# Kernel optimization log

Measured on AMD Instinct MI355X. Metric: run time of the kernel, lower is better.

## Reference

```python
import jax, jax.numpy as jnp
import numpy as np

H = 128; L = 4; N_TOTAL = 2500; M = 4; K = 12
S = N_TOTAL * M          # 10000 subgraphs
F = S * K                # 120000 flat nodes
E_INTRA = 2 * F          # 240000 intra-subgraph edges
E_INTER = 16 * N_TOTAL   # 40000 canonical edges
B = 50; VOCAB = 119; MAX_DIST = 32; BN_EPS = 1e-5


def _bn(x, g, b):
    # training-mode BatchNorm1d over rows (biased var, eps=1e-5)
    mu = x.mean(0)
    var = x.var(0)
    return (x - mu) * jax.lax.rsqrt(var + BN_EPS) * g + b


def _gine(x, ei, ea, W1, b1, W2, b2):
    # PyG GINEConv, eps=0: MLP(x + sum_{src->dst} relu(x[src] + e))
    msg = jax.nn.relu(x[ei[0]] + ea)                              # [E,H]
    agg = jax.ops.segment_sum(msg, ei[1], num_segments=x.shape[0])
    h = x + agg
    return jax.nn.relu(h @ W1 + b1) @ W2 + b2


def setup_inputs():
    key = jax.random.key(0)
    ks = list(jax.random.split(key, 32)); it = iter(ks)
    nk = lambda: next(it)
    rn = lambda shape, s=0.05: jax.random.normal(nk(), shape, dtype=jnp.float32) * s
    x_tok = jax.random.randint(nk(), (F,), 0, VOCAB)
    dist = jax.random.randint(nk(), (F,), 0, MAX_DIST + 1)
    node_ids = jax.random.randint(nk(), (F,), 0, N_TOTAL)
    node_ids = jnp.where(jax.random.uniform(nk(), (F,)) < 0.1, -1, node_ids)
    root_flat_idx = jnp.arange(S) * K
    node_ids = node_ids.at[root_flat_idx].set(jnp.arange(S) // M)  # root = canonical node
    valid = node_ids >= 0
    sub_batch = jnp.repeat(jnp.arange(S), K)
    src = jax.random.randint(nk(), (E_INTRA,), 0, F)
    dst = (src // K) * K + jax.random.randint(nk(), (E_INTRA,), 0, K)  # stay inside subgraph
    intra_ei = jnp.stack([src, dst])
    edge_index = jax.random.randint(nk(), (2, E_INTER), 0, N_TOTAL)
    batch_ids = jnp.arange(N_TOTAL) // (N_TOTAL // B)
    lp = -jax.random.uniform(nk(), (S,)) * 3.0                    # log-probs <= 0
    z = lambda *shape: jnp.zeros(shape, jnp.float32)
    o = lambda *shape: jnp.ones(shape, jnp.float32)
    return dict(
        x_tok=x_tok, dist=dist, node_ids=node_ids, valid=valid,
        sub_batch=sub_batch, root_flat_idx=root_flat_idx,
        intra_ei=intra_ei, edge_index=edge_index, batch_ids=batch_ids,
        lp=lp, ea_flat=rn((E_INTRA, H)), edge_attr=rn((E_INTER, H)),
        atom_emb=rn((VOCAB, H)), dist_emb=rn((MAX_DIST + 1, H)),
        logp_w=rn((1, H)), logp_b=z(H),
        intra_W1=rn((L, H, H)), intra_b1=z(L, H),
        intra_W2=rn((L, H, H)), intra_b2=z(L, H),
        intra_bn_g=o(L, H), intra_bn_b=z(L, H),
        self_W=rn((L, H, H)), self_b=z(L, H),
        root_W=rn((L, H, H)), root_b=z(L, H),
        inter_W1=rn((L, H, H)), inter_b1=z(L, H),
        inter_W2=rn((L, H, H)), inter_b2=z(L, H),
        inter_bn_g=o(L, H), inter_bn_b=z(L, H),
        readout_bn_g=o(H), readout_bn_b=z(H),
        alpha_pool=o(1), alpha_inter=o(1),
    )


def reference(x_tok, dist, node_ids, valid, sub_batch, root_flat_idx, intra_ei,
              edge_index, batch_ids, lp, ea_flat, edge_attr, atom_emb, dist_emb,
              logp_w, logp_b, intra_W1, intra_b1, intra_W2, intra_b2,
              intra_bn_g, intra_bn_b, self_W, self_b, root_W, root_b,
              inter_W1, inter_b1, inter_W2, inter_b2, inter_bn_g, inter_bn_b,
              readout_bn_g, readout_bn_b, alpha_pool, alpha_inter):
    valid_f = valid.astype(jnp.float32)[:, None]                  # [F,1]
    is_root_f = jnp.zeros((F, 1), jnp.float32).at[root_flat_idx].set(1.0)
    clamped_ids = jnp.maximum(node_ids, 0)
    # input encoding: atom embedding + BFS-distance PE + log-prob PE
    logp_pe = jax.nn.relu(lp[sub_batch][:, None] * logp_w[0] + logp_b)
    h = (atom_emb[x_tok] + dist_emb[dist] + logp_pe) * valid_f
    # HT inter-root weights, normalized per canonical root id
    root_ids = node_ids[root_flat_idx]                            # [S]
    rv = root_ids >= 0
    rid = jnp.maximum(root_ids, 0)
    w_un = jnp.where(rv, jnp.exp(-alpha_inter[0] * lp), 0.0)
    w_sum = jax.ops.segment_sum(w_un, rid, num_segments=N_TOTAL)
    ht_w = jnp.where(rv, w_un / (w_sum[rid] + 1e-16), 0.0)        # [S]
    for l in range(L):
        h1 = _gine(h, intra_ei, ea_flat, intra_W1[l], intra_b1[l], intra_W2[l], intra_b2[l])
        h1 = _bn(h1, intra_bn_g[l], intra_bn_b[l]) * valid_f
        h_root_bcast = h[sub_batch * K]
        h_non_root = (h @ self_W[l] + self_b[l]) + (h_root_bcast @ root_W[l] + root_b[l])
        # HT-weighted scatter of root reps to canonical nodes
        h_roots = h[root_flat_idx]                                # [S,H]
        h_root_canon = jax.ops.segment_sum(h_roots * ht_w[:, None], rid, num_segments=N_TOTAL)
        h_inter = _gine(h_root_canon, edge_index, edge_attr, inter_W1[l], inter_b1[l], inter_W2[l], inter_b2[l])
        h_inter = _bn(h_inter, inter_bn_g[l], inter_bn_b[l])
        h_inter_bcast = h_inter[clamped_ids] * valid_f
        out = is_root_f * (h1 + h_inter_bcast) + (1.0 - is_root_f) * (h1 + h_non_root)
        h = jax.nn.relu(out) * valid_f                            # dropout p=0
    # HT softmax readout over the m subgraphs of each canonical node
    h_sub = jax.ops.segment_sum(h * valid_f, sub_batch, num_segments=S)
    h_sub_2d = h_sub.reshape(N_TOTAL, M, H)
    w = jax.nn.softmax(-alpha_pool[0] * lp.reshape(N_TOTAL, M), axis=1)
    node_emb = jnp.einsum('nm,nmh->nh', w, h_sub_2d)
    node_emb = _bn(node_emb, readout_bn_g, readout_bn_b)
    return jax.ops.segment_sum(node_emb, batch_ids, num_segments=B)  # [B,H]
```

## Files before the change

### kernel.cpp

```cpp
#include <hip/hip_runtime.h>
#include <math.h>

#define H 128
#define H4 (H/4)
#define KK 12
#define MSUB 4
#define FF 120000
#define SS 10000
#define NN 2500
#define NBATCH 50
#define NLAYER 4
#define EINTRA 240000
#define EINTER 40000
#define HH (H*H)
#define BN_EPS 1e-5f
#define CAP_I 32
#define CAP_E 96

typedef short short8 __attribute__((ext_vector_type(8)));
typedef float floatx4 __attribute__((ext_vector_type(4)));

__device__ __forceinline__ unsigned short f2bf_rne(float x){
  unsigned u = __float_as_uint(x);
  unsigned r = u + 0x7FFFu + ((u >> 16) & 1u);
  return (unsigned short)(r >> 16);
}


__global__ void k_zero(float* __restrict__ p, int n){
  int i = blockIdx.x*256 + threadIdx.x;
  if (i < n) p[i] = 0.f;
}

__global__ void k_zeroi(int* __restrict__ p, int n){
  int i = blockIdx.x*256 + threadIdx.x;
  if (i < n) p[i] = 0;
}


__global__ void k_bucket(const int* __restrict__ dst, int E, int* __restrict__ cnt,
                         int* __restrict__ beid, int cap){
  int e = blockIdx.x*256 + threadIdx.x;
  if (e >= E) return;
  int d = dst[e];
  int p = atomicAdd(&cnt[d], 1);
  if (p < cap) beid[(size_t)d*cap + p] = e;
}

__global__ void k_scan(const int* __restrict__ cnt, int rows, int cap,
                       int* __restrict__ rowptr, int* __restrict__ gcount){
  __shared__ int sdata[256];
  __shared__ int sbase;
  int tid = threadIdx.x;
  int r = blockIdx.x*256 + tid;
  int v = 0;
  if (r < rows){ v = cnt[r]; if (v > cap) v = cap; }
  sdata[tid] = v;
  __syncthreads();
  for (int ofs = 1; ofs < 256; ofs <<= 1){
    int t = (tid >= ofs) ? sdata[tid-ofs] : 0;
    __syncthreads();
    sdata[tid] += t;
    __syncthreads();
  }
  if (tid == 255) sbase = atomicAdd(gcount, sdata[255]);
  __syncthreads();
  if (r < rows) rowptr[r] = sbase + sdata[tid] - v;
}

__global__ void k_csr_fill(const int* __restrict__ cnt, const int* __restrict__ rowptr,
                           const int* __restrict__ beid, const int* __restrict__ src,
                           int rows, int cap, int2* __restrict__ es){
  int f = blockIdx.x*256 + threadIdx.x;
  if (f >= rows) return;
  int n = cnt[f]; if (n > cap) n = cap;
  int base = rowptr[f];
  const int* bl = beid + (size_t)f*cap;
  for (int i = 0; i < n; ++i){
    int e = bl[i];
    es[base + i] = make_int2(e, src[e]);
  }
}


__global__ void k_encode(float* __restrict__ h, const int* __restrict__ xtok,
                         const int* __restrict__ dist, const int* __restrict__ nids,
                         const int* __restrict__ subb, const float* __restrict__ lp,
                         const float* __restrict__ aemb, const float* __restrict__ demb,
                         const float* __restrict__ lw, const float* __restrict__ lb){
  int idx = blockIdx.x*256 + threadIdx.x;
  if (idx >= FF*H4) return;
  int f = idx >> 5; int c = (idx & 31) << 2;
  float vf = (nids[f] >= 0) ? 1.f : 0.f;
  float l = lp[subb[f]];
  float4 a = *(const float4*)(aemb + (size_t)xtok[f]*H + c);
  float4 d = *(const float4*)(demb + (size_t)dist[f]*H + c);
  float4 w = *(const float4*)(lw + c);
  float4 b = *(const float4*)(lb + c);
  float4 o;
  o.x = (a.x + d.x + fmaxf(fmaf(l, w.x, b.x), 0.f)) * vf;
  o.y = (a.y + d.y + fmaxf(fmaf(l, w.y, b.y), 0.f)) * vf;
  o.z = (a.z + d.z + fmaxf(fmaf(l, w.z, b.z), 0.f)) * vf;
  o.w = (a.w + d.w + fmaxf(fmaf(l, w.w, b.w), 0.f)) * vf;
  *(float4*)(h + (size_t)f*H + c) = o;
}


__global__ void k_htw(const int* __restrict__ nids, const int* __restrict__ rfi,
                      const float* __restrict__ lp, const float* __restrict__ alpha,
                      float* __restrict__ htw){
  int n = blockIdx.x*256 + threadIdx.x;
  if (n >= NN) return;
  float a = alpha[0];
  float w[MSUB]; float sum = 0.f;
  #pragma unroll
  for (int m = 0; m < MSUB; ++m){
    int s = n*MSUB + m;
    int rid = nids[rfi[s]];
    float wm = (rid >= 0) ? expf(-a*lp[s]) : 0.f;
    w[m] = wm; sum += wm;
  }
  float inv = 1.f / (sum + 1e-16f);
  #pragma unroll
  for (int m = 0; m < MSUB; ++m) htw[n*MSUB + m] = w[m]*inv;
}


__global__ void k_gine_gather2(float* __restrict__ outa, const float* __restrict__ x,
                               const float* __restrict__ ea, const int* __restrict__ cnt,
                               const int* __restrict__ rowptr, const int2* __restrict__ es,
                               int rows, int cap){
  int idx = blockIdx.x*256 + threadIdx.x;
  if (idx >= rows*H4) return;
  int f = idx >> 5; int c = (idx & 31) << 2;
  float4 acc = *(const float4*)(x + (size_t)f*H + c);
  int n = cnt[f]; if (n > cap) n = cap;
  const int2* p = es + rowptr[f];
  int i = 0;
  for (; i + 2 <= n; i += 2){
    int2 e0 = p[i];
    int2 e1 = p[i+1];
    float4 x0 = *(const float4*)(x + (size_t)e0.y*H + c);
    float4 a0 = *(const float4*)(ea + (size_t)e0.x*H + c);
    float4 x1 = *(const float4*)(x + (size_t)e1.y*H + c);
    float4 a1 = *(const float4*)(ea + (size_t)e1.x*H + c);
    acc.x += fmaxf(x0.x + a0.x, 0.f) + fmaxf(x1.x + a1.x, 0.f);
    acc.y += fmaxf(x0.y + a0.y, 0.f) + fmaxf(x1.y + a1.y, 0.f);
    acc.z += fmaxf(x0.z + a0.z, 0.f) + fmaxf(x1.z + a1.z, 0.f);
    acc.w += fmaxf(x0.w + a0.w, 0.f) + fmaxf(x1.w + a1.w, 0.f);
  }
  if (i < n){
    int2 e0 = p[i];
    float4 x0 = *(const float4*)(x + (size_t)e0.y*H + c);
    float4 a0 = *(const float4*)(ea + (size_t)e0.x*H + c);
    acc.x += fmaxf(x0.x + a0.x, 0.f);
    acc.y += fmaxf(x0.y + a0.y, 0.f);
    acc.z += fmaxf(x0.z + a0.z, 0.f);
    acc.w += fmaxf(x0.w + a0.w, 0.f);
  }
  *(float4*)(outa + (size_t)f*H + c) = acc;
}


__global__ void k_canon(float* __restrict__ canon, const float* __restrict__ h,
                        const float* __restrict__ htw, const int* __restrict__ rfi){
  int idx = blockIdx.x*256 + threadIdx.x;
  if (idx >= NN*H4) return;
  int n = idx >> 5; int c = (idx & 31) << 2;
  float4 acc = make_float4(0.f,0.f,0.f,0.f);
  #pragma unroll
  for (int m = 0; m < MSUB; ++m){
    int s = n*MSUB + m;
    float w = htw[s];
    const float* p = h + (size_t)rfi[s]*H + c;
    acc.x += w*p[0]; acc.y += w*p[1]; acc.z += w*p[2]; acc.w += w*p[3];
  }
  *(float4*)(canon + (size_t)n*H + c) = acc;
}


__global__ __launch_bounds__(256, 2) void k_mm_mfma(
    const float* __restrict__ in, float* __restrict__ out, int rows,
    const float* __restrict__ W, const float* __restrict__ bias,
    int do_relu, const int* __restrict__ gather)
{
  __shared__ __align__(16) short wfrag[2][4][8][64][8];
  int tid = threadIdx.x;
  int w = tid >> 6, l = tid & 63;
  int quad = l >> 4, n15 = l & 15;

  #pragma unroll
  for (int i = 0; i < 8; ++i){
    int c = w + (i << 2);
    int ks = c >> 3, nt = c & 7;
    #pragma unroll
    for (int j = 0; j < 8; ++j){
      int k = ks*32 + quad*8 + j;
      int n = nt*16 + n15;
      float v = W[(size_t)k*H + n];
      unsigned short hb = f2bf_rne(v);
      float hf = __uint_as_float((unsigned)hb << 16);
      unsigned short lb = f2bf_rne(v - hf);
      wfrag[0][ks][nt][l][j] = (short)hb;
      wfrag[1][ks][nt][l][j] = (short)lb;
    }
  }
  __syncthreads();

  int ngroups = (rows + 63) >> 6;
  for (int g = blockIdx.x; g < ngroups; g += gridDim.x){
    int rload = g*64 + w*16 + n15;
    bool okload = rload < rows;
    int ir = okload ? (gather ? gather[rload] : rload) : 0;
    const float* ap = in + (size_t)ir*H + quad*8;

    short8 ah[4], al[4];
    #pragma unroll
    for (int ks = 0; ks < 4; ++ks){
      float4 a0 = okload ? *(const float4*)(ap + ks*32 + 0) : make_float4(0.f,0.f,0.f,0.f);
      float4 a1 = okload ? *(const float4*)(ap + ks*32 + 4) : make_float4(0.f,0.f,0.f,0.f);
      float av[8] = {a0.x,a0.y,a0.z,a0.w,a1.x,a1.y,a1.z,a1.w};
      #pragma unroll
      for (int j = 0; j < 8; ++j){
        unsigned short hb = f2bf_rne(av[j]);
        float hf = __uint_as_float((unsigned)hb << 16);
        ah[ks][j] = (short)hb;
        al[ks][j] = (short)f2bf_rne(av[j] - hf);
      }
    }

    floatx4 acc[8] = {};
    #pragma unroll
    for (int ks = 0; ks < 4; ++ks){
      #pragma unroll
      for (int nt = 0; nt < 8; ++nt){
        short8 bh = *(const short8*)&wfrag[0][ks][nt][l][0];
        short8 bl = *(const short8*)&wfrag[1][ks][nt][l][0];
        acc[nt] = __builtin_amdgcn_mfma_f32_16x16x32_bf16(ah[ks], bh, acc[nt], 0, 0, 0);
        acc[nt] = __builtin_amdgcn_mfma_f32_16x16x32_bf16(al[ks], bh, acc[nt], 0, 0, 0);
        acc[nt] = __builtin_amdgcn_mfma_f32_16x16x32_bf16(ah[ks], bl, acc[nt], 0, 0, 0);
      }
    }

    int rbase = g*64 + w*16 + quad*4;
    #pragma unroll
    for (int nt = 0; nt < 8; ++nt){
      int col = nt*16 + n15;
      float bv = bias[col];
      #pragma unroll
      for (int reg = 0; reg < 4; ++reg){
        int r = rbase + reg;
        if (r < rows){
          float v = acc[nt][reg] + bv;
          if (do_relu) v = fmaxf(v, 0.f);
          out[(size_t)r*H + col] = v;
        }
      }
    }
  }
}


__global__ __launch_bounds__(256, 2) void k_mm_mfma_stats(
    const float* __restrict__ in, float* __restrict__ out, int rows,
    const float* __restrict__ W, const float* __restrict__ bias,
    double* __restrict__ stats)
{
  __shared__ __align__(16) short wfrag[2][4][8][64][8];
  int tid = threadIdx.x;
  int w = tid >> 6, l = tid & 63;
  int quad = l >> 4, n15 = l & 15;

  #pragma unroll
  for (int i = 0; i < 8; ++i){
    int c = w + (i << 2);
    int ks = c >> 3, nt = c & 7;
    #pragma unroll
    for (int j = 0; j < 8; ++j){
      int k = ks*32 + quad*8 + j;
      int n = nt*16 + n15;
      float v = W[(size_t)k*H + n];
      unsigned short hb = f2bf_rne(v);
      float hf = __uint_as_float((unsigned)hb << 16);
      unsigned short lb = f2bf_rne(v - hf);
      wfrag[0][ks][nt][l][j] = (short)hb;
      wfrag[1][ks][nt][l][j] = (short)lb;
    }
  }
  __syncthreads();

  double s0[8] = {0,0,0,0,0,0,0,0};
  double s1[8] = {0,0,0,0,0,0,0,0};

  int ngroups = (rows + 63) >> 6;
  for (int g = blockIdx.x; g < ngroups; g += gridDim.x){
    int rload = g*64 + w*16 + n15;
    bool okload = rload < rows;
    const float* ap = in + (size_t)(okload ? rload : 0)*H + quad*8;

    short8 ah[4], al[4];
    #pragma unroll
    for (int ks = 0; ks < 4; ++ks){
      float4 a0 = okload ? *(const float4*)(ap + ks*32 + 0) : make_float4(0.f,0.f,0.f,0.f);
      float4 a1 = okload ? *(const float4*)(ap + ks*32 + 4) : make_float4(0.f,0.f,0.f,0.f);
      float av[8] = {a0.x,a0.y,a0.z,a0.w,a1.x,a1.y,a1.z,a1.w};
      #pragma unroll
      for (int j = 0; j < 8; ++j){
        unsigned short hb = f2bf_rne(av[j]);
        float hf = __uint_as_float((unsigned)hb << 16);
        ah[ks][j] = (short)hb;
        al[ks][j] = (short)f2bf_rne(av[j] - hf);
      }
    }

    floatx4 acc[8] = {};
    #pragma unroll
    for (int ks = 0; ks < 4; ++ks){
      #pragma unroll
      for (int nt = 0; nt < 8; ++nt){
        short8 bh = *(const short8*)&wfrag[0][ks][nt][l][0];
        short8 bl = *(const short8*)&wfrag[1][ks][nt][l][0];
        acc[nt] = __builtin_amdgcn_mfma_f32_16x16x32_bf16(ah[ks], bh, acc[nt], 0, 0, 0);
        acc[nt] = __builtin_amdgcn_mfma_f32_16x16x32_bf16(al[ks], bh, acc[nt], 0, 0, 0);
        acc[nt] = __builtin_amdgcn_mfma_f32_16x16x32_bf16(ah[ks], bl, acc[nt], 0, 0, 0);
      }
    }

    int rbase = g*64 + w*16 + quad*4;
    #pragma unroll
    for (int nt = 0; nt < 8; ++nt){
      int col = nt*16 + n15;
      float bv = bias[col];
      #pragma unroll
      for (int reg = 0; reg < 4; ++reg){
        int r = rbase + reg;
        if (r < rows){
          float v = acc[nt][reg] + bv;
          out[(size_t)r*H + col] = v;
          s0[nt] += (double)v;
          s1[nt] += (double)v * (double)v;
        }
      }
    }
  }

  #pragma unroll
  for (int nt = 0; nt < 8; ++nt){
    double a = s0[nt], b = s1[nt];
    a += __shfl_xor(a, 16, 64); b += __shfl_xor(b, 16, 64);
    a += __shfl_xor(a, 32, 64); b += __shfl_xor(b, 32, 64);
    if (quad == 0){
      int col = nt*16 + n15;
      atomicAdd(&stats[col], a);
      atomicAdd(&stats[H+col], b);
    }
  }
}


__global__ void k_bnstats(const float* __restrict__ x, int rows, double* __restrict__ stats){
  int g = blockIdx.x*256 + threadIdx.x;
  int c = g & (H-1);
  int rstart = g >> 7;
  int rstride = (gridDim.x*256) >> 7;
  double s = 0.0, s2 = 0.0;
  for (int r = rstart; r < rows; r += rstride){
    float v = x[(size_t)r*H + c];
    s += v; s2 += (double)v*(double)v;
  }
  atomicAdd(&stats[c], s);
  atomicAdd(&stats[H+c], s2);
}

__global__ void k_bnfin(double* __restrict__ stats, int rows, float* __restrict__ muinv){
  int c = threadIdx.x;
  if (c < H){
    double mu = stats[c] / (double)rows;
    double var = stats[H+c] / (double)rows - mu*mu;
    muinv[c]   = (float)mu;
    muinv[H+c] = (float)(1.0 / sqrt(var + (double)BN_EPS));
    stats[c] = 0.0; stats[H+c] = 0.0;
  }
}

__global__ void k_bnapply(float* __restrict__ x, const float* __restrict__ muinv,
                          const float* __restrict__ g, const float* __restrict__ b, int rows){
  int idx = blockIdx.x*256 + threadIdx.x;
  if (idx >= rows*H4) return;
  int r = idx >> 5; int c = (idx & 31) << 2;
  float4 v  = *(const float4*)(x + (size_t)r*H + c);
  float4 mu = *(const float4*)(muinv + c);
  float4 iv = *(const float4*)(muinv + H + c);
  float4 gg = *(const float4*)(g + c);
  float4 bb = *(const float4*)(b + c);
  v.x = (v.x-mu.x)*iv.x*gg.x + bb.x;
  v.y = (v.y-mu.y)*iv.y*gg.y + bb.y;
  v.z = (v.z-mu.z)*iv.z*gg.z + bb.z;
  v.w = (v.w-mu.w)*iv.w*gg.w + bb.w;
  *(float4*)(x + (size_t)r*H + c) = v;
}


__global__ void k_combine(float* __restrict__ h, const float* __restrict__ h1raw,
                          const float* __restrict__ r1, const float* __restrict__ r2,
                          const float* __restrict__ hinter, const float* __restrict__ muinv,
                          const float* __restrict__ bg, const float* __restrict__ bb,
                          const int* __restrict__ nids){
  int idx = blockIdx.x*256 + threadIdx.x;
  if (idx >= FF*H4) return;
  int f = idx >> 5; int c = (idx & 31) << 2;
  int nid = nids[f];
  float vf = (nid >= 0) ? 1.f : 0.f;
  int cid = (nid < 0) ? 0 : nid;
  float4 x  = *(const float4*)(h1raw + (size_t)f*H + c);
  float4 mu = *(const float4*)(muinv + c);
  float4 iv = *(const float4*)(muinv + H + c);
  float4 g4 = *(const float4*)(bg + c);
  float4 b4 = *(const float4*)(bb + c);
  float4 h1;
  h1.x = ((x.x-mu.x)*iv.x*g4.x + b4.x) * vf;
  h1.y = ((x.y-mu.y)*iv.y*g4.y + b4.y) * vf;
  h1.z = ((x.z-mu.z)*iv.z*g4.z + b4.z) * vf;
  h1.w = ((x.w-mu.w)*iv.w*g4.w + b4.w) * vf;
  float4 o;
  if (f % KK == 0){
    float4 hi = *(const float4*)(hinter + (size_t)cid*H + c);
    o.x = h1.x + hi.x*vf; o.y = h1.y + hi.y*vf; o.z = h1.z + hi.z*vf; o.w = h1.w + hi.w*vf;
  } else {
    float4 a  = *(const float4*)(r1 + (size_t)f*H + c);
    float4 rr = *(const float4*)(r2 + (size_t)(f/KK)*H + c);
    o.x = h1.x + a.x + rr.x; o.y = h1.y + a.y + rr.y; o.z = h1.z + a.z + rr.z; o.w = h1.w + a.w + rr.w;
  }
  o.x = fmaxf(o.x,0.f)*vf; o.y = fmaxf(o.y,0.f)*vf; o.z = fmaxf(o.z,0.f)*vf; o.w = fmaxf(o.w,0.f)*vf;
  *(float4*)(h + (size_t)f*H + c) = o;
}


__global__ void k_hsub(float* __restrict__ hsub, const float* __restrict__ h){
  int idx = blockIdx.x*256 + threadIdx.x;
  if (idx >= SS*H4) return;
  int s = idx >> 5; int c = (idx & 31) << 2;
  float4 acc = make_float4(0.f,0.f,0.f,0.f);
  const float* base = h + (size_t)s*KK*H + c;
  #pragma unroll
  for (int k = 0; k < KK; ++k){
    float4 v = *(const float4*)(base + (size_t)k*H);
    acc.x += v.x; acc.y += v.y; acc.z += v.z; acc.w += v.w;
  }
  *(float4*)(hsub + (size_t)s*H + c) = acc;
}

__global__ void k_poolw(float* __restrict__ poolw, const float* __restrict__ lp,
                        const float* __restrict__ alpha){
  int n = blockIdx.x*256 + threadIdx.x;
  if (n >= NN) return;
  float a = alpha[0];
  float s0 = -a*lp[n*MSUB+0], s1 = -a*lp[n*MSUB+1], s2 = -a*lp[n*MSUB+2], s3 = -a*lp[n*MSUB+3];
  float m = fmaxf(fmaxf(s0,s1), fmaxf(s2,s3));
  float e0 = expf(s0-m), e1 = expf(s1-m), e2 = expf(s2-m), e3 = expf(s3-m);
  float sum = e0+e1+e2+e3;
  poolw[n*MSUB+0] = e0/sum; poolw[n*MSUB+1] = e1/sum;
  poolw[n*MSUB+2] = e2/sum; poolw[n*MSUB+3] = e3/sum;
}

__global__ void k_nodeemb(float* __restrict__ nemb, const float* __restrict__ hsub,
                          const float* __restrict__ poolw){
  int idx = blockIdx.x*256 + threadIdx.x;
  if (idx >= NN*H4) return;
  int n = idx >> 5; int c = (idx & 31) << 2;
  float w0 = poolw[n*MSUB+0], w1 = poolw[n*MSUB+1], w2 = poolw[n*MSUB+2], w3 = poolw[n*MSUB+3];
  const float* base = hsub + (size_t)n*MSUB*H + c;
  float4 v0 = *(const float4*)(base + 0*H);
  float4 v1 = *(const float4*)(base + 1*H);
  float4 v2 = *(const float4*)(base + 2*H);
  float4 v3 = *(const float4*)(base + 3*H);
  float4 o;
  o.x = w0*v0.x + w1*v1.x + w2*v2.x + w3*v3.x;
  o.y = w0*v0.y + w1*v1.y + w2*v2.y + w3*v3.y;
  o.z = w0*v0.z + w1*v1.z + w2*v2.z + w3*v3.z;
  o.w = w0*v0.w + w1*v1.w + w2*v2.w + w3*v3.w;
  *(float4*)(nemb + (size_t)n*H + c) = o;
}

__global__ void k_out(float* __restrict__ out, const float* __restrict__ nemb,
                      const float* __restrict__ muinv, const float* __restrict__ g,
                      const float* __restrict__ b){
  int idx = blockIdx.x*256 + threadIdx.x;
  if (idx >= NBATCH*H) return;
  int bi = idx >> 7; int c = idx & (H-1);
  float mu = muinv[c], iv = muinv[H+c], gg = g[c], bb = b[c];
  float acc = 0.f;
  const float* base = nemb + (size_t)bi*(NN/NBATCH)*H + c;
  for (int i = 0; i < NN/NBATCH; ++i)
    acc += (base[(size_t)i*H] - mu)*iv*gg + bb;
  out[idx] = acc;
}


extern "C" void kernel_launch(void* const* d_in, const int* in_sizes, int n_in,
                              void* d_out, int out_size, void* d_ws, size_t ws_size,
                              hipStream_t stream) {
  const int*   x_tok      = (const int*)  d_in[0];
  const int*   dist       = (const int*)  d_in[1];
  const int*   node_ids   = (const int*)  d_in[2];
  const int*   sub_batch  = (const int*)  d_in[4];
  const int*   rfi        = (const int*)  d_in[5];
  const int*   intra_ei   = (const int*)  d_in[6];
  const int*   edge_index = (const int*)  d_in[7];
  const float* lp         = (const float*)d_in[9];
  const float* ea_flat    = (const float*)d_in[10];
  const float* edge_attr  = (const float*)d_in[11];
  const float* atom_emb   = (const float*)d_in[12];
  const float* dist_emb   = (const float*)d_in[13];
  const float* logp_w     = (const float*)d_in[14];
  const float* logp_b     = (const float*)d_in[15];
  const float* intra_W1   = (const float*)d_in[16];
  const float* intra_b1   = (const float*)d_in[17];
  const float* intra_W2   = (const float*)d_in[18];
  const float* intra_b2   = (const float*)d_in[19];
  const float* intra_bn_g = (const float*)d_in[20];
  const float* intra_bn_b = (const float*)d_in[21];
  const float* self_W     = (const float*)d_in[22];
  const float* self_b     = (const float*)d_in[23];
  const float* root_W     = (const float*)d_in[24];
  const float* root_b     = (const float*)d_in[25];
  const float* inter_W1   = (const float*)d_in[26];
  const float* inter_b1   = (const float*)d_in[27];
  const float* inter_W2   = (const float*)d_in[28];
  const float* inter_b2   = (const float*)d_in[29];
  const float* inter_bn_g = (const float*)d_in[30];
  const float* inter_bn_b = (const float*)d_in[31];
  const float* ro_bn_g    = (const float*)d_in[32];
  const float* ro_bn_b    = (const float*)d_in[33];
  const float* alpha_pool = (const float*)d_in[34];
  const float* alpha_inter= (const float*)d_in[35];

  const int* isrc = intra_ei;
  const int* idst = intra_ei + EINTRA;
  const int* esrc = edge_index;
  const int* edst = edge_index + EINTER;

  float* out = (float*)d_out;

  char* ws = (char*)d_ws;
  size_t off = 0;
  auto nxt = [&](size_t bytes) -> void* {
    void* p = ws + off;
    off += (bytes + 255) & ~(size_t)255;
    return p;
  };
  float*  h      = (float*) nxt((size_t)FF*H*4);
  float*  hmid   = (float*) nxt((size_t)FF*H*4);
  float*  tbuf   = (float*) nxt((size_t)FF*H*4);
  float*  r2     = (float*) nxt((size_t)SS*H*4);
  float*  canon  = (float*) nxt((size_t)NN*H*4);
  float*  agg2   = (float*) nxt((size_t)NN*H*4);
  float*  hsub   = (float*) nxt((size_t)SS*H*4);
  float*  nemb   = (float*) nxt((size_t)NN*H*4);
  float*  htw    = (float*) nxt((size_t)SS*4);
  float*  poolw  = (float*) nxt((size_t)NN*MSUB*4);
  double* statsA = (double*)nxt((size_t)2*H*8);
  double* statsB = (double*)nxt((size_t)2*H*8);
  float*  muinvA = (float*) nxt((size_t)2*H*4);
  float*  muinvB = (float*) nxt((size_t)2*H*4);
  int*    icnt   = (int*)   nxt((size_t)FF*4);
  int*    ibeid  = (int*)   nxt((size_t)FF*CAP_I*4);
  int*    ecnt   = (int*)   nxt((size_t)NN*4);
  int*    ebeid  = (int*)   nxt((size_t)NN*CAP_E*4);
  int*    irow   = (int*)   nxt((size_t)FF*4);
  int*    erow   = (int*)   nxt((size_t)NN*4);
  int2*   ies    = (int2*)  nxt((size_t)EINTRA*8);
  int2*   ees    = (int2*)  nxt((size_t)EINTER*8);
  int*    gcnt   = (int*)   nxt((size_t)2*4);
  (void)ws_size; (void)n_in; (void)in_sizes; (void)out_size; (void)sub_batch;

  const int G_FH4 = FF*H4/256;
  const int G_SH4 = SS*H4/256;
  const int G_NH4 = (NN*H4 + 255)/256;
  const int G_N   = (NN + 255)/256;
  const int G_F   = (FF + 255)/256;
  const int G_MM_F = 512;
  const int G_MM_S = (SS + 63)/64;
  const int G_MM_N = (NN + 63)/64;

  k_zero<<<2, 256, 0, stream>>>((float*)statsA, 2*H*2);
  k_zero<<<2, 256, 0, stream>>>((float*)statsB, 2*H*2);
  k_zeroi<<<G_F, 256, 0, stream>>>(icnt, FF);
  k_zeroi<<<G_N, 256, 0, stream>>>(ecnt, NN);
  k_zeroi<<<1, 256, 0, stream>>>(gcnt, 2);

  k_bucket<<<(EINTRA+255)/256, 256, 0, stream>>>(idst, EINTRA, icnt, ibeid, CAP_I);
  k_bucket<<<(EINTER+255)/256, 256, 0, stream>>>(edst, EINTER, ecnt, ebeid, CAP_E);
  k_scan<<<G_F, 256, 0, stream>>>(icnt, FF, CAP_I, irow, gcnt);
  k_scan<<<G_N, 256, 0, stream>>>(ecnt, NN, CAP_E, erow, gcnt+1);
  k_csr_fill<<<G_F, 256, 0, stream>>>(icnt, irow, ibeid, isrc, FF, CAP_I, ies);
  k_csr_fill<<<G_N, 256, 0, stream>>>(ecnt, erow, ebeid, esrc, NN, CAP_E, ees);

  k_encode<<<G_FH4, 256, 0, stream>>>(h, x_tok, dist, node_ids, sub_batch, lp,
                                      atom_emb, dist_emb, logp_w, logp_b);
  k_htw<<<G_N, 256, 0, stream>>>(node_ids, rfi, lp, alpha_inter, htw);

  for (int l = 0; l < NLAYER; ++l){
    const float* W1 = intra_W1 + (size_t)l*HH; const float* b1 = intra_b1 + (size_t)l*H;
    const float* W2 = intra_W2 + (size_t)l*HH; const float* b2 = intra_b2 + (size_t)l*H;

    k_gine_gather2<<<G_FH4, 256, 0, stream>>>(hmid, h, ea_flat, icnt, irow, ies, FF, CAP_I);
    k_mm_mfma<<<G_MM_F, 256, 0, stream>>>(hmid, tbuf, FF, W1, b1, 1, nullptr);
    k_mm_mfma_stats<<<G_MM_F, 256, 0, stream>>>(tbuf, hmid, FF, W2, b2, statsA);
    k_bnfin<<<1, 128, 0, stream>>>(statsA, FF, muinvA);

    k_canon<<<G_NH4, 256, 0, stream>>>(canon, h, htw, rfi);
    k_mm_mfma<<<G_MM_S, 256, 0, stream>>>(h, r2, SS, root_W + (size_t)l*HH,
                                          root_b + (size_t)l*H, 0, rfi);

    k_gine_gather2<<<G_NH4, 256, 0, stream>>>(agg2, canon, edge_attr, ecnt, erow, ees, NN, CAP_E);
    k_mm_mfma<<<G_MM_N, 256, 0, stream>>>(agg2, tbuf, NN, inter_W1 + (size_t)l*HH,
                                          inter_b1 + (size_t)l*H, 1, nullptr);
    k_mm_mfma<<<G_MM_N, 256, 0, stream>>>(tbuf, agg2, NN, inter_W2 + (size_t)l*HH,
                                          inter_b2 + (size_t)l*H, 0, nullptr);
    k_bnstats<<<128, 256, 0, stream>>>(agg2, NN, statsB);
    k_bnfin<<<1, 128, 0, stream>>>(statsB, NN, muinvB);
    k_bnapply<<<G_NH4, 256, 0, stream>>>(agg2, muinvB, inter_bn_g + (size_t)l*H,
                                         inter_bn_b + (size_t)l*H, NN);

    k_mm_mfma<<<G_MM_F, 256, 0, stream>>>(h, tbuf, FF, self_W + (size_t)l*HH,
                                          self_b + (size_t)l*H, 0, nullptr);
    k_combine<<<G_FH4, 256, 0, stream>>>(h, hmid, tbuf, r2, agg2, muinvA,
                                         intra_bn_g + (size_t)l*H,
                                         intra_bn_b + (size_t)l*H, node_ids);
  }

  k_hsub<<<G_SH4, 256, 0, stream>>>(hsub, h);
  k_poolw<<<G_N, 256, 0, stream>>>(poolw, lp, alpha_pool);
  k_nodeemb<<<G_NH4, 256, 0, stream>>>(nemb, hsub, poolw);
  k_bnstats<<<128, 256, 0, stream>>>(nemb, NN, statsB);
  k_bnfin<<<1, 128, 0, stream>>>(statsB, NN, muinvB);
  k_out<<<(NBATCH*H+255)/256, 256, 0, stream>>>(out, nemb, muinvB, ro_bn_g, ro_bn_b);
}
```

Before: 1.981 ms.

## Prefetch next row tile in MFMA matmuls and replace BN stat atomics with partials

The MFMA matmul kernels now load the next row group's A operand into registers while the current group is converted and multiplied, a software-pipelined prefetch meant to hide global load latency. BatchNorm statistics are no longer accumulated with double atomics. Each block writes per-block partial sums, reduced in shared memory in the stats matmul, and a single finalize kernel sums them, which also removes the zeroing kernels. This adds register pressure (8 float4 prefetch registers) that may hurt occupancy, plus a larger partials buffer.

```diff
diff --git a/kernel.cpp b/kernel.cpp
--- a/kernel.cpp
+++ b/kernel.cpp
@@ -26,11 +26,6 @@
   return (unsigned short)(r >> 16);
 }
 
-
-__global__ void k_zero(float* __restrict__ p, int n){
-  int i = blockIdx.x*256 + threadIdx.x;
-  if (i < n) p[i] = 0.f;
-}
 
 __global__ void k_zeroi(int* __restrict__ p, int n){
   int i = blockIdx.x*256 + threadIdx.x;
@@ -179,6 +174,34 @@
 }
 
 
+__device__ __forceinline__ void load_a_raw(const float* __restrict__ in, int rows, int rload,
+                                           const int* __restrict__ gather, int quad, float4* ra){
+  bool ok = rload < rows;
+  int ir = ok ? (gather ? gather[rload] : rload) : 0;
+  const float* ap = in + (size_t)ir*H + quad*8;
+  #pragma unroll
+  for (int ks = 0; ks < 4; ++ks){
+    ra[ks*2+0] = ok ? *(const float4*)(ap + ks*32 + 0) : make_float4(0.f,0.f,0.f,0.f);
+    ra[ks*2+1] = ok ? *(const float4*)(ap + ks*32 + 4) : make_float4(0.f,0.f,0.f,0.f);
+  }
+}
+
+__device__ __forceinline__ void conv_a(const float4* ra, short8* ah, short8* al){
+  #pragma unroll
+  for (int ks = 0; ks < 4; ++ks){
+    float av[8] = {ra[ks*2].x, ra[ks*2].y, ra[ks*2].z, ra[ks*2].w,
+                   ra[ks*2+1].x, ra[ks*2+1].y, ra[ks*2+1].z, ra[ks*2+1].w};
+    #pragma unroll
+    for (int j = 0; j < 8; ++j){
+      unsigned short hb = f2bf_rne(av[j]);
+      float hf = __uint_as_float((unsigned)hb << 16);
+      ah[ks][j] = (short)hb;
+      al[ks][j] = (short)f2bf_rne(av[j] - hf);
+    }
+  }
+}
+
+
 __global__ __launch_bounds__(256, 2) void k_mm_mfma(
     const float* __restrict__ in, float* __restrict__ out, int rows,
     const float* __restrict__ W, const float* __restrict__ bias,
@@ -208,26 +231,14 @@
   __syncthreads();
 
   int ngroups = (rows + 63) >> 6;
-  for (int g = blockIdx.x; g < ngroups; g += gridDim.x){
-    int rload = g*64 + w*16 + n15;
-    bool okload = rload < rows;
-    int ir = okload ? (gather ? gather[rload] : rload) : 0;
-    const float* ap = in + (size_t)ir*H + quad*8;
-
+  int g = blockIdx.x;
+  float4 ra[8];
+  if (g < ngroups) load_a_raw(in, rows, g*64 + w*16 + n15, gather, quad, ra);
+  while (g < ngroups){
+    int gn = g + gridDim.x;
     short8 ah[4], al[4];
-    #pragma unroll
-    for (int ks = 0; ks < 4; ++ks){
-      float4 a0 = okload ? *(const float4*)(ap + ks*32 + 0) : make_float4(0.f,0.f,0.f,0.f);
-      float4 a1 = okload ? *(const float4*)(ap + ks*32 + 4) : make_float4(0.f,0.f,0.f,0.f);
-      float av[8] = {a0.x,a0.y,a0.z,a0.w,a1.x,a1.y,a1.z,a1.w};
-      #pragma unroll
-      for (int j = 0; j < 8; ++j){
-        unsigned short hb = f2bf_rne(av[j]);
-        float hf = __uint_as_float((unsigned)hb << 16);
-        ah[ks][j] = (short)hb;
-        al[ks][j] = (short)f2bf_rne(av[j] - hf);
-      }
-    }
+    conv_a(ra, ah, al);
+    if (gn < ngroups) load_a_raw(in, rows, gn*64 + w*16 + n15, gather, quad, ra);
 
     floatx4 acc[8] = {};
     #pragma unroll
@@ -257,6 +268,7 @@
         }
       }
     }
+    g = gn;
   }
 }
 
@@ -264,7 +276,7 @@
 __global__ __launch_bounds__(256, 2) void k_mm_mfma_stats(
     const float* __restrict__ in, float* __restrict__ out, int rows,
     const float* __restrict__ W, const float* __restrict__ bias,
-    double* __restrict__ stats)
+    double* __restrict__ part)
 {
   __shared__ __align__(16) short wfrag[2][4][8][64][8];
   int tid = threadIdx.x;
@@ -293,25 +305,14 @@
   double s1[8] = {0,0,0,0,0,0,0,0};
 
   int ngroups = (rows + 63) >> 6;
-  for (int g = blockIdx.x; g < ngroups; g += gridDim.x){
-    int rload = g*64 + w*16 + n15;
-    bool okload = rload < rows;
-    const float* ap = in + (size_t)(okload ? rload : 0)*H + quad*8;
-
+  int g = blockIdx.x;
+  float4 ra[8];
+  if (g < ngroups) load_a_raw(in, rows, g*64 + w*16 + n15, nullptr, quad, ra);
+  while (g < ngroups){
+    int gn = g + gridDim.x;
     short8 ah[4], al[4];
-    #pragma unroll
-    for (int ks = 0; ks < 4; ++ks){
-      float4 a0 = okload ? *(const float4*)(ap + ks*32 + 0) : make_float4(0.f,0.f,0.f,0.f);
-      float4 a1 = okload ? *(const float4*)(ap + ks*32 + 4) : make_float4(0.f,0.f,0.f,0.f);
-      float av[8] = {a0.x,a0.y,a0.z,a0.w,a1.x,a1.y,a1.z,a1.w};
-      #pragma unroll
-      for (int j = 0; j < 8; ++j){
-        unsigned short hb = f2bf_rne(av[j]);
-        float hf = __uint_as_float((unsigned)hb << 16);
-        ah[ks][j] = (short)hb;
-        al[ks][j] = (short)f2bf_rne(av[j] - hf);
-      }
-    }
+    conv_a(ra, ah, al);
+    if (gn < ngroups) load_a_raw(in, rows, gn*64 + w*16 + n15, nullptr, quad, ra);
 
     floatx4 acc[8] = {};
     #pragma unroll
@@ -342,8 +343,11 @@
         }
       }
     }
-  }
-
+    g = gn;
+  }
+
+  __syncthreads();
+  double* red = (double*)&wfrag[0][0][0][0][0];
   #pragma unroll
   for (int nt = 0; nt < 8; ++nt){
     double a = s0[nt], b = s1[nt];
@@ -351,35 +355,51 @@
     a += __shfl_xor(a, 32, 64); b += __shfl_xor(b, 32, 64);
     if (quad == 0){
       int col = nt*16 + n15;
-      atomicAdd(&stats[col], a);
-      atomicAdd(&stats[H+col], b);
-    }
-  }
-}
-
-
-__global__ void k_bnstats(const float* __restrict__ x, int rows, double* __restrict__ stats){
+      red[(size_t)(w*2+0)*H + col] = a;
+      red[(size_t)(w*2+1)*H + col] = b;
+    }
+  }
+  __syncthreads();
+  if (tid < H){
+    int col = tid;
+    double a = red[0*H+col] + red[2*H+col] + red[4*H+col] + red[6*H+col];
+    double b = red[1*H+col] + red[3*H+col] + red[5*H+col] + red[7*H+col];
+    part[(size_t)(blockIdx.x*2+0)*H + col] = a;
+    part[(size_t)(blockIdx.x*2+1)*H + col] = b;
+  }
+}
+
+
+__global__ void k_bnstats_p(const float* __restrict__ x, int rows, double* __restrict__ part){
   int g = blockIdx.x*256 + threadIdx.x;
   int c = g & (H-1);
-  int rstart = g >> 7;
-  int rstride = (gridDim.x*256) >> 7;
-  double s = 0.0, s2 = 0.0;
-  for (int r = rstart; r < rows; r += rstride){
+  int s = g >> 7;
+  int stride = (gridDim.x*256) >> 7;
+  double a = 0.0, b = 0.0;
+  for (int r = s; r < rows; r += stride){
     float v = x[(size_t)r*H + c];
-    s += v; s2 += (double)v*(double)v;
-  }
-  atomicAdd(&stats[c], s);
-  atomicAdd(&stats[H+c], s2);
-}
-
-__global__ void k_bnfin(double* __restrict__ stats, int rows, float* __restrict__ muinv){
-  int c = threadIdx.x;
-  if (c < H){
-    double mu = stats[c] / (double)rows;
-    double var = stats[H+c] / (double)rows - mu*mu;
+    a += v; b += (double)v*(double)v;
+  }
+  part[(size_t)(s*2+0)*H + c] = a;
+  part[(size_t)(s*2+1)*H + c] = b;
+}
+
+__global__ void k_bnfin_p(const double* __restrict__ part, int nstreams, int rows,
+                          float* __restrict__ muinv){
+  __shared__ double sh[2][H];
+  int tid = threadIdx.x;
+  int c = tid & (H-1);
+  int which = tid >> 7;
+  double s = 0.0;
+  for (int i = 0; i < nstreams; ++i)
+    s += part[(size_t)(i*2+which)*H + c];
+  sh[which][c] = s;
+  __syncthreads();
+  if (tid < H){
+    double mu = sh[0][c] / (double)rows;
+    double var = sh[1][c] / (double)rows - mu*mu;
     muinv[c]   = (float)mu;
     muinv[H+c] = (float)(1.0 / sqrt(var + (double)BN_EPS));
-    stats[c] = 0.0; stats[H+c] = 0.0;
   }
 }
 
@@ -549,6 +569,11 @@
     off += (bytes + 255) & ~(size_t)255;
     return p;
   };
+  const int G_MM_F = 512;
+  const int G_MM_S = (SS + 63)/64;
+  const int G_MM_N = (NN + 63)/64;
+  const int G_BN_S = 32;
+
   float*  h      = (float*) nxt((size_t)FF*H*4);
   float*  hmid   = (float*) nxt((size_t)FF*H*4);
   float*  tbuf   = (float*) nxt((size_t)FF*H*4);
@@ -559,8 +584,8 @@
   float*  nemb   = (float*) nxt((size_t)NN*H*4);
   float*  htw    = (float*) nxt((size_t)SS*4);
   float*  poolw  = (float*) nxt((size_t)NN*MSUB*4);
-  double* statsA = (double*)nxt((size_t)2*H*8);
-  double* statsB = (double*)nxt((size_t)2*H*8);
+  double* statsA = (double*)nxt((size_t)G_MM_F*2*H*8);
+  double* statsB = (double*)nxt((size_t)(G_BN_S*2)*2*H*8);
   float*  muinvA = (float*) nxt((size_t)2*H*4);
   float*  muinvB = (float*) nxt((size_t)2*H*4);
   int*    icnt   = (int*)   nxt((size_t)FF*4);
@@ -579,12 +604,7 @@
   const int G_NH4 = (NN*H4 + 255)/256;
   const int G_N   = (NN + 255)/256;
   const int G_F   = (FF + 255)/256;
-  const int G_MM_F = 512;
-  const int G_MM_S = (SS + 63)/64;
-  const int G_MM_N = (NN + 63)/64;
-
-  k_zero<<<2, 256, 0, stream>>>((float*)statsA, 2*H*2);
-  k_zero<<<2, 256, 0, stream>>>((float*)statsB, 2*H*2);
+
   k_zeroi<<<G_F, 256, 0, stream>>>(icnt, FF);
   k_zeroi<<<G_N, 256, 0, stream>>>(ecnt, NN);
   k_zeroi<<<1, 256, 0, stream>>>(gcnt, 2);
@@ -607,7 +627,7 @@
     k_gine_gather2<<<G_FH4, 256, 0, stream>>>(hmid, h, ea_flat, icnt, irow, ies, FF, CAP_I);
     k_mm_mfma<<<G_MM_F, 256, 0, stream>>>(hmid, tbuf, FF, W1, b1, 1, nullptr);
     k_mm_mfma_stats<<<G_MM_F, 256, 0, stream>>>(tbuf, hmid, FF, W2, b2, statsA);
-    k_bnfin<<<1, 128, 0, stream>>>(statsA, FF, muinvA);
+    k_bnfin_p<<<1, 256, 0, stream>>>(statsA, G_MM_F, FF, muinvA);
 
     k_canon<<<G_NH4, 256, 0, stream>>>(canon, h, htw, rfi);
     k_mm_mfma<<<G_MM_S, 256, 0, stream>>>(h, r2, SS, root_W + (size_t)l*HH,
@@ -618,8 +638,8 @@
                                           inter_b1 + (size_t)l*H, 1, nullptr);
     k_mm_mfma<<<G_MM_N, 256, 0, stream>>>(tbuf, agg2, NN, inter_W2 + (size_t)l*HH,
                                           inter_b2 + (size_t)l*H, 0, nullptr);
-    k_bnstats<<<128, 256, 0, stream>>>(agg2, NN, statsB);
-    k_bnfin<<<1, 128, 0, stream>>>(statsB, NN, muinvB);
+    k_bnstats_p<<<G_BN_S, 256, 0, stream>>>(agg2, NN, statsB);
+    k_bnfin_p<<<1, 256, 0, stream>>>(statsB, G_BN_S*2, NN, muinvB);
     k_bnapply<<<G_NH4, 256, 0, stream>>>(agg2, muinvB, inter_bn_g + (size_t)l*H,
                                          inter_bn_b + (size_t)l*H, NN);
 
@@ -633,7 +653,7 @@
   k_hsub<<<G_SH4, 256, 0, stream>>>(hsub, h);
   k_poolw<<<G_N, 256, 0, stream>>>(poolw, lp, alpha_pool);
   k_nodeemb<<<G_NH4, 256, 0, stream>>>(nemb, hsub, poolw);
-  k_bnstats<<<128, 256, 0, stream>>>(nemb, NN, statsB);
-  k_bnfin<<<1, 128, 0, stream>>>(statsB, NN, muinvB);
+  k_bnstats_p<<<G_BN_S, 256, 0, stream>>>(nemb, NN, statsB);
+  k_bnfin_p<<<1, 256, 0, stream>>>(statsB, G_BN_S*2, NN, muinvB);
   k_out<<<(NBATCH*H+255)/256, 256, 0, stream>>>(out, nemb, muinvB, ro_bn_g, ro_bn_b);
 }
```

Measured after the change: 2.510 ms. 1.27x slower.
